# Kernel optimization log

Hardware: AMD Instinct MI355X
Metric: run time of the kernel (lower is better)

## Reference

```python
import jax, jax.numpy as jnp
import numpy as np

B, S, E, H = 1, 2048, 1024, 16
D = E // H
HEAVY_RATIO, RECENT_RATIO, PENALTY = 0.1, 0.1, 0.99
NEG = jnp.finfo(jnp.float32).min


def heavy_hitter_mask(attn, heavy_budget, recent_budget, penalty):
    # attn: [N, S, S] pre-softmax scores (with causal mask already added)
    N, Sq, _ = attn.shape
    cb = heavy_budget + recent_budget  # cache budget
    cols = jnp.arange(Sq)
    tmp = jax.nn.softmax(attn.astype(jnp.float32), axis=-1)
    # exponential penalty factor: penalty ** (cb-1, cb-2, ..., 0)
    pf = penalty ** (jnp.arange(cb, 0, -1).astype(jnp.float32) - 1.0)
    acc = jnp.einsum('nts,t->ns', tmp[:, :cb, :], pf)  # accumulated attention score [N,S]
    acc = acc * (cols < cb).astype(jnp.float32)        # zero beyond cache budget
    prev0 = jnp.broadcast_to(cols < cb, (N, Sq))       # mask_bottom row cb-1 (pre-tril)
    rows = jnp.swapaxes(attn[:, cb:, :], 0, 1)         # time-major [T,N,S]
    toks = jnp.arange(cb, Sq)

    def step(carry, inp):
        acc, prev = carry
        row, tok = inp
        li = tok - recent_budget                       # local_index
        in_local = (cols < li)[None, :]
        acc = jnp.where(in_local, acc * prev.astype(jnp.float32), acc)
        scores = jnp.where(in_local, acc, -jnp.inf)
        _, idx = jax.lax.top_k(scores, heavy_budget)   # heavy hitters [N,k]
        heavy = jnp.zeros((N, Sq), bool).at[jnp.arange(N)[:, None], idx].set(True)
        mask_row = heavy | (cols >= li)[None, :]
        p = jax.nn.softmax(jnp.where(mask_row, row.astype(jnp.float32), NEG), axis=-1)
        acc = acc * penalty + p
        # carry pre-tril row (matches torch loop); emit tril'd row
        return (acc, mask_row), mask_row & (cols <= tok)[None, :]

    (_, _), out_rows = jax.lax.scan(step, (acc, prev0), (rows, toks))
    # first cb rows: all-True cb x cb block, then tril -> causal within block
    top = jnp.broadcast_to((cols[None, :] <= jnp.arange(cb)[:, None])[None], (N, cb, Sq))
    return jnp.concatenate([top, jnp.swapaxes(out_rows, 0, 1)], axis=1)


def _forward(hidden_states, attention_mask, Wq, bq, Wk, bk, Wv, bv, Wo, bo):
    scaling = D ** -0.5
    q = (hidden_states @ Wq.T + bq) * scaling
    k = hidden_states @ Wk.T + bk
    v = hidden_states @ Wv.T + bv

    def shp(x):
        return x.reshape(B, S, H, D).transpose(0, 2, 1, 3).reshape(B * H, S, D)

    q, k, v = shp(q), shp(k), shp(v)
    attn = jnp.einsum('nsd,ntd->nst', q, k)                    # [B*H,S,S]
    attn = attn.reshape(B, H, S, S) + attention_mask
    attn = jnp.maximum(attn, NEG).reshape(B * H, S, S)
    hb = int(HEAVY_RATIO * S)
    rb = int(RECENT_RATIO * S)
    mask = heavy_hitter_mask(attn, hb, rb, PENALTY)
    attn = jnp.where(mask, attn, jnp.min(attention_mask))
    probs = jax.nn.softmax(attn.astype(jnp.float32), axis=-1)
    out = jnp.einsum('nst,ntd->nsd', probs, v)
    out = out.reshape(B, H, S, D).transpose(0, 2, 1, 3).reshape(B, S, E)
    return out @ Wo.T + bo


def setup_inputs() -> dict:
    key = jax.random.key(0)
    ks = jax.random.split(key, 9)
    hidden_states = jax.random.normal(ks[0], (B, S, E), jnp.float32)
    cols = jnp.arange(S)
    causal = (cols[None, :] <= cols[:, None])
    attention_mask = jnp.where(causal, 0.0, NEG)[None, None].astype(jnp.float32)
    attention_mask = jnp.broadcast_to(attention_mask, (B, 1, S, S)) + jnp.zeros((B, 1, S, S), jnp.float32)
    lin = lambda k: jax.random.normal(k, (E, E), jnp.float32) * 0.02
    return {
        'hidden_states': hidden_states,
        'attention_mask': attention_mask,
        'Wq': lin(ks[1]), 'bq': jnp.zeros((E,), jnp.float32),
        'Wk': lin(ks[2]), 'bk': jnp.zeros((E,), jnp.float32),
        'Wv': lin(ks[3]), 'bv': jnp.zeros((E,), jnp.float32),
        'Wo': lin(ks[4]), 'bo': jnp.zeros((E,), jnp.float32),
    }


def reference(hidden_states, attention_mask, Wq, bq, Wk, bk, Wv, bv, Wo, bo):
    return _forward(hidden_states, attention_mask, Wq, bq, Wk, bk, Wv, bv, Wo, bo)
```

## Files before the change

### kernel.cpp

```cpp
#include <hip/hip_runtime.h>

#define S_ 2048
#define E_ 1024
#define H_ 16
#define D_ 64
#define HB_ 204
#define RB_ 204
#define CB_ 408
#define NSCAN_ (S_ - CB_)
#define PEN_ 0.99f
#define NEGINF (-__builtin_huge_valf())
#define POSINF (__builtin_huge_valf())

typedef unsigned short u16;
typedef unsigned int u32;
typedef unsigned int u32x4 __attribute__((ext_vector_type(4)));

__device__ __forceinline__ float bf2f(u16 u) {
    union { u32 u; float f; } a; a.u = ((u32)u) << 16; return a.f;
}
__device__ __forceinline__ u16 f2bf(float f) {
    union { float f; u32 u; } a; a.f = f;
    u32 r = (a.u + 0x7FFFu + ((a.u >> 16) & 1u)) >> 16;
    return (u16)r;
}

#define DPPF(ID, V, CTRL, RMASK) \
    __int_as_float(__builtin_amdgcn_update_dpp(__float_as_int(ID), __float_as_int(V), CTRL, RMASK, 0xf, false))

__device__ __forceinline__ float wsum64_63(float v) {
    float t;
    t = DPPF(0.f, v, 0x111, 0xf); v += t;
    t = DPPF(0.f, v, 0x112, 0xf); v += t;
    t = DPPF(0.f, v, 0x114, 0xf); v += t;
    t = DPPF(0.f, v, 0x118, 0xf); v += t;
    t = DPPF(0.f, v, 0x142, 0xa); v += t;
    t = DPPF(0.f, v, 0x143, 0xc); v += t;
    return v;
}
__device__ __forceinline__ float wsum64(float v) {
    v = wsum64_63(v);
    return __int_as_float(__builtin_amdgcn_readlane(__float_as_int(v), 63));
}
template <int CTRL, int RMASK>
__device__ __forceinline__ double dmin_step(double v) {
    const int lo = __double2loint(v), hi = __double2hiint(v);
    const int slo = __builtin_amdgcn_update_dpp(0, lo, CTRL, RMASK, 0xf, false);
    const int shi = __builtin_amdgcn_update_dpp(0x7FF00000, hi, CTRL, RMASK, 0xf, false);
    return fmin(v, __hiloint2double(shi, slo));
}
__device__ __forceinline__ double wmind64(double v) {
    v = dmin_step<0x111, 0xf>(v);
    v = dmin_step<0x112, 0xf>(v);
    v = dmin_step<0x114, 0xf>(v);
    v = dmin_step<0x118, 0xf>(v);
    v = dmin_step<0x142, 0xa>(v);
    v = dmin_step<0x143, 0xc>(v);
    return v;
}

__global__ __launch_bounds__(256) void qkv_gemm(
    const float* __restrict__ X,
    const float* __restrict__ W0, const float* __restrict__ b0,
    const float* __restrict__ W1, const float* __restrict__ b1,
    const float* __restrict__ W2, const float* __restrict__ b2,
    float* __restrict__ Q, float* __restrict__ K, float* __restrict__ V)
{
    const int z = blockIdx.z;
    const float* W    = (z == 0) ? W0 : (z == 1) ? W1 : W2;
    const float* bias = (z == 0) ? b0 : (z == 1) ? b1 : b2;
    float* dst        = (z == 0) ? Q  : (z == 1) ? K  : V;
    const int o0 = blockIdx.x * 128, s0 = blockIdx.y * 128;
    __shared__ float As[16][132];
    __shared__ float Bs[16][132];
    const int tid = threadIdx.x;
    const int ty = tid >> 4, tx = tid & 15;
    const int r = tid >> 1, kq = (tid & 1) << 3;
    float acc[8][8] = {};
    for (int kb = 0; kb < E_; kb += 16) {
        float4 a0 = *(const float4*)&X[(size_t)(s0 + r) * E_ + kb + kq];
        float4 a1 = *(const float4*)&X[(size_t)(s0 + r) * E_ + kb + kq + 4];
        float4 w0 = *(const float4*)&W[(size_t)(o0 + r) * E_ + kb + kq];
        float4 w1 = *(const float4*)&W[(size_t)(o0 + r) * E_ + kb + kq + 4];
        __syncthreads();
        As[kq+0][r]=a0.x; As[kq+1][r]=a0.y; As[kq+2][r]=a0.z; As[kq+3][r]=a0.w;
        As[kq+4][r]=a1.x; As[kq+5][r]=a1.y; As[kq+6][r]=a1.z; As[kq+7][r]=a1.w;
        Bs[kq+0][r]=w0.x; Bs[kq+1][r]=w0.y; Bs[kq+2][r]=w0.z; Bs[kq+3][r]=w0.w;
        Bs[kq+4][r]=w1.x; Bs[kq+5][r]=w1.y; Bs[kq+6][r]=w1.z; Bs[kq+7][r]=w1.w;
        __syncthreads();
        #pragma unroll
        for (int kk = 0; kk < 16; ++kk) {
            float av[8], bv[8];
            *(float4*)&av[0] = *(const float4*)&As[kk][ty * 8];
            *(float4*)&av[4] = *(const float4*)&As[kk][ty * 8 + 4];
            *(float4*)&bv[0] = *(const float4*)&Bs[kk][tx * 8];
            *(float4*)&bv[4] = *(const float4*)&Bs[kk][tx * 8 + 4];
            #pragma unroll
            for (int i = 0; i < 8; ++i)
                #pragma unroll
                for (int j = 0; j < 8; ++j) acc[i][j] += av[i] * bv[j];
        }
    }
    #pragma unroll
    for (int i = 0; i < 8; ++i) {
        const int s = s0 + ty * 8 + i;
        #pragma unroll
        for (int jq = 0; jq < 2; ++jq) {
            const int o = o0 + tx * 8 + jq * 4;
            float4 v;
            v.x = acc[i][jq*4+0] + bias[o+0];
            v.y = acc[i][jq*4+1] + bias[o+1];
            v.z = acc[i][jq*4+2] + bias[o+2];
            v.w = acc[i][jq*4+3] + bias[o+3];
            if (z == 0) { v.x *= 0.125f; v.y *= 0.125f; v.z *= 0.125f; v.w *= 0.125f; }
            *(float4*)&dst[((size_t)(o >> 6) * S_ + s) * D_ + (o & 63)] = v;
        }
    }
}

__global__ __launch_bounds__(256) void proj_gemm(
    const float* __restrict__ X, const float* __restrict__ W,
    const float* __restrict__ bias, float* __restrict__ Y)
{
    const int o0 = blockIdx.x * 128, s0 = blockIdx.y * 128;
    __shared__ float As[16][132];
    __shared__ float Bs[16][132];
    const int tid = threadIdx.x;
    const int ty = tid >> 4, tx = tid & 15;
    const int r = tid >> 1, kq = (tid & 1) << 3;
    float acc[8][8] = {};
    for (int kb = 0; kb < E_; kb += 16) {
        float4 a0 = *(const float4*)&X[(size_t)(s0 + r) * E_ + kb + kq];
        float4 a1 = *(const float4*)&X[(size_t)(s0 + r) * E_ + kb + kq + 4];
        float4 w0 = *(const float4*)&W[(size_t)(o0 + r) * E_ + kb + kq];
        float4 w1 = *(const float4*)&W[(size_t)(o0 + r) * E_ + kb + kq + 4];
        __syncthreads();
        As[kq+0][r]=a0.x; As[kq+1][r]=a0.y; As[kq+2][r]=a0.z; As[kq+3][r]=a0.w;
        As[kq+4][r]=a1.x; As[kq+5][r]=a1.y; As[kq+6][r]=a1.z; As[kq+7][r]=a1.w;
        Bs[kq+0][r]=w0.x; Bs[kq+1][r]=w0.y; Bs[kq+2][r]=w0.z; Bs[kq+3][r]=w0.w;
        Bs[kq+4][r]=w1.x; Bs[kq+5][r]=w1.y; Bs[kq+6][r]=w1.z; Bs[kq+7][r]=w1.w;
        __syncthreads();
        #pragma unroll
        for (int kk = 0; kk < 16; ++kk) {
            float av[8], bv[8];
            *(float4*)&av[0] = *(const float4*)&As[kk][ty * 8];
            *(float4*)&av[4] = *(const float4*)&As[kk][ty * 8 + 4];
            *(float4*)&bv[0] = *(const float4*)&Bs[kk][tx * 8];
            *(float4*)&bv[4] = *(const float4*)&Bs[kk][tx * 8 + 4];
            #pragma unroll
            for (int i = 0; i < 8; ++i)
                #pragma unroll
                for (int j = 0; j < 8; ++j) acc[i][j] += av[i] * bv[j];
        }
    }
    #pragma unroll
    for (int i = 0; i < 8; ++i) {
        const int s = s0 + ty * 8 + i;
        #pragma unroll
        for (int jq = 0; jq < 2; ++jq) {
            const int o = o0 + tx * 8 + jq * 4;
            float4 v;
            v.x = acc[i][jq*4+0] + bias[o+0];
            v.y = acc[i][jq*4+1] + bias[o+1];
            v.z = acc[i][jq*4+2] + bias[o+2];
            v.w = acc[i][jq*4+3] + bias[o+3];
            *(float4*)&Y[(size_t)s * E_ + o] = v;
        }
    }
}

__global__ __launch_bounds__(256) void sc_gemm(const float* __restrict__ Q,
                                               const float* __restrict__ K,
                                               u16* __restrict__ Sc)
{
    const int h = blockIdx.z;
    const int jt = blockIdx.x, it = blockIdx.y;
    if (jt > it) return;
    const int i0 = it * 64, j0 = jt * 64;
    __shared__ float Qs[64][65];
    __shared__ float Ks[64][65];
    const float* Qh = Q + (size_t)h * S_ * D_;
    const float* Kh = K + (size_t)h * S_ * D_;
    const int tid = threadIdx.x;
    for (int idx = tid; idx < 1024; idx += 256) {
        const int rr = idx >> 4, c4 = (idx & 15) << 2;
        float4 q4 = *(const float4*)&Qh[(size_t)(i0 + rr) * D_ + c4];
        Qs[c4 + 0][rr] = q4.x; Qs[c4 + 1][rr] = q4.y; Qs[c4 + 2][rr] = q4.z; Qs[c4 + 3][rr] = q4.w;
        float4 k4 = *(const float4*)&Kh[(size_t)(j0 + rr) * D_ + c4];
        Ks[c4 + 0][rr] = k4.x; Ks[c4 + 1][rr] = k4.y; Ks[c4 + 2][rr] = k4.z; Ks[c4 + 3][rr] = k4.w;
    }
    __syncthreads();
    const int ty = tid >> 4, tx = tid & 15;
    float acc[4][4] = {};
    #pragma unroll 4
    for (int kk = 0; kk < 64; ++kk) {
        float4 a4 = *(const float4*)&Qs[kk][ty * 4];
        float4 b4 = *(const float4*)&Ks[kk][tx * 4];
        const float av[4] = {a4.x, a4.y, a4.z, a4.w};
        const float bv[4] = {b4.x, b4.y, b4.z, b4.w};
        #pragma unroll
        for (int i = 0; i < 4; ++i)
            #pragma unroll
            for (int j = 0; j < 4; ++j) acc[i][j] += av[i] * bv[j];
    }
    u16* out = Sc + ((size_t)h * S_ + i0) * S_ + j0;
    #pragma unroll
    for (int i = 0; i < 4; ++i)
        #pragma unroll
        for (int j = 0; j < 4; ++j)
            out[(size_t)(ty * 4 + i) * S_ + tx * 4 + j] = f2bf(acc[i][j]);
}

__global__ __launch_bounds__(256) void prep_kernel(const u16* __restrict__ Sc,
                                                   float* __restrict__ rsumG,
                                                   float* __restrict__ accG)
{
    const int h = blockIdx.y;
    const int wave = threadIdx.x >> 6, lane = threadIdx.x & 63;
    const int bx = blockIdx.x;
    if (bx < NSCAN_ / 4) {
        const int tok = CB_ + bx * 4 + wave;
        const u16* row = Sc + ((size_t)h * S_ + tok) * S_ + (tok - RB_);
        float sm = 0.f;
        #pragma unroll
        for (int k = 0; k < 4; ++k) {
            const int j = k * 64 + lane;
            if (j <= RB_) sm += __expf(bf2f(row[j]));
        }
        const float z = wsum64(sm);
        if (lane == 0) rsumG[(size_t)h * NSCAN_ + tok - CB_] = z;
    } else {
        const int t = (bx - NSCAN_ / 4) * 4 + wave;
        const u16* row = Sc + ((size_t)h * S_ + t) * S_;
        float sm = 0.f;
        for (int c = lane; c <= t; c += 64) sm += __expf(bf2f(row[c]));
        const float z = wsum64(sm);
        const float w = __powf(PEN_, (float)(CB_ - 1 - t)) / z;
        for (int c = lane; c <= t; c += 64)
            atomicAdd(&accG[h * CB_ + c], __expf(bf2f(row[c])) * w);
    }
}

#define NFULL_ (CB_ * H_)
#define NPART_ (NSCAN_ * H_)

__global__ __launch_bounds__(256) void scan_fill(const u16* __restrict__ Sc,
                                                 const float* __restrict__ accG,
                                                 const float* __restrict__ rsumG,
                                                 u16* __restrict__ heavyOut,
                                                 const float* __restrict__ V,
                                                 float* __restrict__ O)
{
    __shared__ __align__(16) char ldsPool[15872];
    const int bid = blockIdx.x;
    const int tid = threadIdx.x;

    if (bid >= 16) {
        float* sbuf  = (float*)ldsPool;
        float* wred  = (float*)(ldsPool + 1664);
        float* opart = (float*)(ldsPool + 1696);
        const int lane = tid & 63, wave = tid >> 6;
        int h, r, c0, n;
        bool partial;
        if (bid < 16 + NFULL_) {
            const int t2 = bid - 16;
            r = t2 >> 4; h = t2 & 15;
            c0 = 0; n = r + 1; partial = false;
        } else {
            const int idx = bid - 16 - NFULL_;
            r = CB_ + (idx >> 4); h = idx & 15;
            c0 = r - RB_; n = RB_ + 1; partial = true;
        }
        const u16* srow = Sc + ((size_t)h * S_ + r) * S_;
        float ls = 0.f;
        for (int i = tid; i < n; i += 256) {
            const float p = __expf(bf2f(srow[c0 + i]));
            sbuf[i] = p; ls += p;
        }
        ls = wsum64(ls);
        if (lane == 0) wred[wave] = ls;
        __syncthreads();
        const float Z = wred[0] + wred[1] + wred[2] + wred[3];
        float pv = 0.f;
        const float* vh = V + (size_t)h * S_ * D_;
        for (int i = wave; i < n; i += 4)
            pv += sbuf[i] * vh[(size_t)(c0 + i) * D_ + lane];
        opart[wave * 64 + lane] = pv;
        __syncthreads();
        if (tid < 64) {
            const float tot = opart[tid] + opart[64 + tid] + opart[128 + tid] + opart[192 + tid];
            O[(size_t)r * E_ + h * D_ + tid] = partial ? tot : (tot / Z);
        }
        return;
    }

    __builtin_amdgcn_s_setprio(3);
    const int h = bid;
    const int lane = tid & 63, wv = tid >> 6;
    float*  ring    = (float*)ldsPool;
    float*  rsumLDS = (float*)(ldsPool + 1024);
    u16*    rowbufA = (u16*)(ldsPool + 7584);
    u16*    rowbufB = (u16*)(ldsPool + 11680);
    float*  wredL   = (float*)(ldsPool + 15776);
    double* kredL   = (double*)(ldsPool + 15792);
    float*  eli1L   = (float*)(ldsPool + 15824);
    const u16* sch = Sc + (size_t)h * S_ * S_;
    const float* accH = accG + h * CB_;
    u16* hOutH = heavyOut + (size_t)h * NSCAN_ * HB_;

    const bool vHeavy = (tid < HB_);
    const bool vRing  = (tid <= RB_);
    const bool vCand  = (tid == 255);

    u32x4 p0, p1, p2, p3;
    #define ISSUE1(BUF, ROWI)                                                 \
        do {                                                                  \
            const void* _ap = (const void*)((const char*)(sch + (size_t)(ROWI) * S_) + tid * 16); \
            asm volatile("global_load_dwordx4 %0, %1, off"                    \
                         : "=&v"(BUF) : "v"(_ap) : "memory");                 \
        } while (0)
    #define WAIT_VM(N) asm volatile("s_waitcnt vmcnt(" #N ")" ::: "memory")
    #define SBAR() asm volatile("s_waitcnt lgkmcnt(0)\n\ts_barrier" ::: "memory")

    ISSUE1(p0, CB_ + 0);
    ISSUE1(p1, CB_ + 1);
    ISSUE1(p2, CB_ + 2);
    ISSUE1(p3, CB_ + 3);

    for (int i = tid; i < NSCAN_; i += 256) rsumLDS[i] = rsumG[(size_t)h * NSCAN_ + i];
    for (int c = HB_ + tid; c < CB_; c += 256) ring[c & 255] = accH[c];
    int   hcol = vHeavy ? tid : 0;
    float hacc = vHeavy ? accH[tid] : POSINF;

    __syncthreads();
    ((u32x4*)rowbufA)[tid] = p0;
    __syncthreads();

    {
        ISSUE1(p0, CB_ + 4);
        const u16* srow = rowbufA;
        const float sg = bf2f(srow[hcol]);
        const float e  = vHeavy ? __expf(sg) : 0.f;
        const float ls = wsum64_63(e);
        if (lane == 63) wredL[wv] = ls;
        float oldw = 0.f, expw = 0.f;
        if (vRing) {
            expw = __expf(bf2f(srow[HB_ + tid]));
            oldw = (tid == RB_) ? 0.f : ring[(HB_ + tid) & 255];
        }
        ((u32x4*)rowbufB)[tid] = p1;
        __syncthreads();
        const float4 ws = *(const float4*)wredL;
        const float Z = ws.x + ws.y + ws.z + ws.w + rsumLDS[0];
        const float invZ = __fdividef(1.f, Z);
        hacc = hacc * PEN_ + e * invZ;
        if (vHeavy) hOutH[tid] = (u16)tid;
        if (vRing)  ring[(HB_ + tid) & 255] = oldw * PEN_ + expw * invZ;
        __syncthreads();
    }

    #define SCAN_ITER(TOK, LD, ST, WN, FS)                                       \
    do {                                                                         \
        const int _si_tok = (TOK);                                               \
        const int _si_li  = _si_tok - RB_;                                       \
        const int _si_nr  = (_si_tok + 4 < S_) ? _si_tok + 4 : S_ - 1;           \
        ISSUE1(LD, _si_nr);                                                      \
        const u16* _si_srow = (_si_tok & 1) ? rowbufB : rowbufA;                 \
        const float _si_accc = ring[(_si_li - 1) & 255];      \
        const int   _si_hc = vCand ? (_si_li - 1) : hcol;                        \
        const float _si_ha = vCand ? _si_accc : hacc;                            \
        const float _si_sg = bf2f(_si_srow[_si_hc]);                             \
        float _si_oldw = 0.f, _si_expw = 0.f;                                    \
        if (vRing) {                                                             \
            _si_expw = __expf(bf2f(_si_srow[_si_li + tid]));                     \
            _si_oldw = (tid == RB_) ? 0.f : ring[(_si_li + tid) & 255];          \
        }                                                                        \
        const float _si_rsum = rsumLDS[_si_tok - CB_];                           \
        const float _si_e = (vHeavy || vCand) ? __expf(_si_sg) : 0.f;            \
        const float _si_ls = wsum64_63(_si_e);                                   \
        double _si_key = __hiloint2double(__float_as_int(_si_ha),                \
                                          ((2047 - _si_hc) << 8) | tid);         \
        _si_key = wmind64(_si_key);                                              \
        if (lane == 63) {                                                        \
            wredL[wv] = _si_ls;                                                  \
            kredL[wv] = _si_key;                                                 \
            if (wv == 3) *eli1L = _si_e;                                         \
        }                                                                        \
        if (!(FS)) { WAIT_VM(WN); }                                              \
        ((u32x4*)(((_si_tok + 1) & 1) ? rowbufB : rowbufA))[tid] = (ST);         \
        if (FS) { __syncthreads(); } else { SBAR(); }                            \
        const float4 _si_ws = *(const float4*)wredL;                             \
        const double _si_km = fmin(fmin(kredL[0], kredL[1]),                     \
                                   fmin(kredL[2], kredL[3]));                    \
        const int _si_lo  = __double2loint(_si_km);                              \
        const int _si_ev  = _si_lo & 255;                                        \
        const int _si_hev = 2047 - (_si_lo >> 8);                                \
        const float _si_ebc = __expf(bf2f(_si_srow[_si_hev]));                   \
        const float _si_el1 = *eli1L;                                            \
        const float _si_Z = (_si_ws.x + _si_ws.y + _si_ws.z + _si_ws.w)          \
                            - _si_ebc + _si_rsum;                                \
        const float _si_invZ = __fdividef(1.f, _si_Z);                           \
        const bool _si_m = (tid == _si_ev);                                      \
        hcol = _si_m ? (_si_li - 1) : _si_hc;                                    \
        hacc = (_si_m ? _si_accc : _si_ha) * PEN_                                \
             + (_si_m ? _si_el1 : _si_e) * _si_invZ;                             \
        if (vHeavy) hOutH[(size_t)(_si_tok - CB_) * HB_ + tid] = (u16)hcol;      \
        if (vRing)  ring[(_si_li + tid) & 255] = _si_oldw * PEN_ + _si_expw * _si_invZ; \
        if (FS) { __syncthreads(); } else { SBAR(); }                            \
    } while (0)

    SCAN_ITER(CB_ + 1, p1, p2, 0, 1);
    SCAN_ITER(CB_ + 2, p2, p3, 0, 1);
    SCAN_ITER(CB_ + 3, p3, p0, 0, 1);
    SCAN_ITER(CB_ + 4, p0, p1, 3, 0);
    for (int tokBase = CB_ + 5; tokBase + 3 < S_; tokBase += 4) {
        SCAN_ITER(tokBase + 0, p1, p2, 3, 0);
        SCAN_ITER(tokBase + 1, p2, p3, 3, 0);
        SCAN_ITER(tokBase + 2, p3, p0, 3, 0);
        SCAN_ITER(tokBase + 3, p0, p1, 3, 0);
    }
    SCAN_ITER(S_ - 3, p1, p2, 3, 0);
    SCAN_ITER(S_ - 2, p2, p3, 3, 0);
    SCAN_ITER(S_ - 1, p3, p0, 3, 0);
    #undef SCAN_ITER
    #undef ISSUE1
    #undef WAIT_VM
    #undef SBAR
}

__global__ __launch_bounds__(256) void heavy_merge(const u16* __restrict__ Sc,
                                                   const float* __restrict__ V,
                                                   const u16* __restrict__ heavyIn,
                                                   const float* __restrict__ rsumG,
                                                   float* __restrict__ O)
{
    const int idx = blockIdx.x;
    const int r = CB_ + (idx >> 4), h = idx & 15;
    const int tid = threadIdx.x;
    const int lane = tid & 63, wave = tid >> 6;
    __shared__ float sbuf[208];
    __shared__ u16 cbuf[208];
    __shared__ float wred[4];
    __shared__ float opart[4][64];
    const u16* srow = Sc + ((size_t)h * S_ + r) * S_;
    const u16* hrow = heavyIn + ((size_t)h * NSCAN_ + (r - CB_)) * HB_;
    float ls = 0.f;
    for (int i = tid; i < HB_; i += 256) {
        const int col = hrow[i];
        const float p = __expf(bf2f(srow[col]));
        sbuf[i] = p; cbuf[i] = (u16)col;
        ls += p;
    }
    ls = wsum64(ls);
    if (lane == 0) wred[wave] = ls;
    __syncthreads();
    const float Z = wred[0] + wred[1] + wred[2] + wred[3]
                  + rsumG[(size_t)h * NSCAN_ + r - CB_];
    float pv = 0.f;
    const float* vh = V + (size_t)h * S_ * D_;
    for (int i = wave; i < HB_; i += 4)
        pv += sbuf[i] * vh[(size_t)cbuf[i] * D_ + lane];
    opart[wave][lane] = pv;
    __syncthreads();
    if (tid < 64) {
        const float tot = opart[0][tid] + opart[1][tid] + opart[2][tid] + opart[3][tid];
        float* op = &O[(size_t)r * E_ + h * D_ + tid];
        *op = (*op + tot) / Z;
    }
}

extern "C" void kernel_launch(void* const* d_in, const int* in_sizes, int n_in,
                              void* d_out, int out_size, void* d_ws, size_t ws_size,
                              hipStream_t stream)
{
    const float* hs = (const float*)d_in[0];
    const float* Wq = (const float*)d_in[2];
    const float* bq = (const float*)d_in[3];
    const float* Wk = (const float*)d_in[4];
    const float* bk = (const float*)d_in[5];
    const float* Wv = (const float*)d_in[6];
    const float* bv = (const float*)d_in[7];
    const float* Wo = (const float*)d_in[8];
    const float* bo = (const float*)d_in[9];

    char* ws = (char*)d_ws;
    const size_t MB = 1024 * 1024;
    float* Q     = (float*)(ws);
    float* K     = (float*)(ws + 8 * MB);
    float* V     = (float*)(ws + 16 * MB);
    u16*   Sc    = (u16*)  (ws + 24 * MB);
    u16*   hvy   = (u16*)  (ws + 152 * MB);
    float* rsumG = (float*)(ws + 163 * MB);
    float* accG  = (float*)(ws + 164 * MB);
    float* O     = (float*)(ws + 168 * MB);
    (void)ws_size; (void)in_sizes; (void)n_in; (void)out_size;

    (void)hipMemsetAsync(accG, 0, (size_t)H_ * CB_ * sizeof(float), stream);
    qkv_gemm<<<dim3(8, 16, 3), 256, 0, stream>>>(hs, Wq, bq, Wk, bk, Wv, bv, Q, K, V);
    sc_gemm <<<dim3(32, 32, 16), 256, 0, stream>>>(Q, K, Sc);
    prep_kernel<<<dim3(NSCAN_ / 4 + CB_ / 4, H_), 256, 0, stream>>>(Sc, rsumG, accG);
    scan_fill<<<16 + NFULL_ + NPART_, 256, 0, stream>>>(Sc, accG, rsumG, hvy, V, O);
    heavy_merge<<<NPART_, 256, 0, stream>>>(Sc, V, hvy, rsumG, O);
    proj_gemm<<<dim3(8, 16, 1), 256, 0, stream>>>(O, Wo, bo, (float*)d_out);
}
```

Measured before the change: 1.640 ms.

## Remove second barrier per scan step via triple-buffered rows and parity reduction slots

The sequential heavy-hitter scan now uses three LDS row buffers and two alternating reduction slots, so each token step needs one barrier instead of two. The candidate accumulator for the column leaving the recent window is carried in a register rather than reread from the ring after a barrier, and ring updates are reordered so they cannot race with the next step's reads. This targets barrier latency on the serial critical path of the scan, at the cost of more LDS and subtler ordering that must hold across steps.

Measured after the change: 1.637 ms. About the same (-0.2%).

```diff
diff --git a/kernel.cpp b/kernel.cpp
--- a/kernel.cpp
+++ b/kernel.cpp
@@ -251,7 +251,7 @@
                                                  const float* __restrict__ V,
                                                  float* __restrict__ O)
 {
-    __shared__ __align__(16) char ldsPool[15872];
+    __shared__ __align__(16) char ldsPool[19984];
     const int bid = blockIdx.x;
     const int tid = threadIdx.x;
 
@@ -299,11 +299,12 @@
     const int lane = tid & 63, wv = tid >> 6;
     float*  ring    = (float*)ldsPool;
     float*  rsumLDS = (float*)(ldsPool + 1024);
-    u16*    rowbufA = (u16*)(ldsPool + 7584);
-    u16*    rowbufB = (u16*)(ldsPool + 11680);
-    float*  wredL   = (float*)(ldsPool + 15776);
-    double* kredL   = (double*)(ldsPool + 15792);
-    float*  eli1L   = (float*)(ldsPool + 15824);
+    u16*    buf_0   = (u16*)(ldsPool + 7584);
+    u16*    buf_1   = (u16*)(ldsPool + 11680);
+    u16*    buf_2   = (u16*)(ldsPool + 15776);
+    float*  wredL   = (float*)(ldsPool + 19872);
+    double* kredL   = (double*)(ldsPool + 19904);
+    float*  el1L    = (float*)(ldsPool + 19968);
     const u16* sch = Sc + (size_t)h * S_ * S_;
     const float* accH = accG + h * CB_;
     u16* hOutH = heavyOut + (size_t)h * NSCAN_ * HB_;
@@ -331,14 +332,15 @@
     for (int c = HB_ + tid; c < CB_; c += 256) ring[c & 255] = accH[c];
     int   hcol = vHeavy ? tid : 0;
     float hacc = vHeavy ? accH[tid] : POSINF;
+    float accc;
 
     __syncthreads();
-    ((u32x4*)rowbufA)[tid] = p0;
+    ((u32x4*)buf_0)[tid] = p0;
     __syncthreads();
 
     {
         ISSUE1(p0, CB_ + 4);
-        const u16* srow = rowbufA;
+        const u16* srow = buf_0;
         const float sg = bf2f(srow[hcol]);
         const float e  = vHeavy ? __expf(sg) : 0.f;
         const float ls = wsum64_63(e);
@@ -348,7 +350,7 @@
             expw = __expf(bf2f(srow[HB_ + tid]));
             oldw = (tid == RB_) ? 0.f : ring[(HB_ + tid) & 255];
         }
-        ((u32x4*)rowbufB)[tid] = p1;
+        ((u32x4*)buf_1)[tid] = p1;
         __syncthreads();
         const float4 ws = *(const float4*)wredL;
         const float Z = ws.x + ws.y + ws.z + ws.w + rsumLDS[0];
@@ -357,71 +359,81 @@
         if (vHeavy) hOutH[tid] = (u16)tid;
         if (vRing)  ring[(HB_ + tid) & 255] = oldw * PEN_ + expw * invZ;
         __syncthreads();
-    }
-
-    #define SCAN_ITER(TOK, LD, ST, WN, FS)                                       \
+        accc = ring[HB_ & 255];
+    }
+
+    #define SCAN_ITER(TOK, LD, ST, SB, DB, P)                                    \
     do {                                                                         \
         const int _si_tok = (TOK);                                               \
         const int _si_li  = _si_tok - RB_;                                       \
         const int _si_nr  = (_si_tok + 4 < S_) ? _si_tok + 4 : S_ - 1;           \
         ISSUE1(LD, _si_nr);                                                      \
-        const u16* _si_srow = (_si_tok & 1) ? rowbufB : rowbufA;                 \
-        const float _si_accc = ring[(_si_li - 1) & 255];      \
+        const u16* _si_srow = buf_##SB;                                          \
         const int   _si_hc = vCand ? (_si_li - 1) : hcol;                        \
-        const float _si_ha = vCand ? _si_accc : hacc;                            \
+        const float _si_ha = vCand ? accc : hacc;                                \
         const float _si_sg = bf2f(_si_srow[_si_hc]);                             \
-        float _si_oldw = 0.f, _si_expw = 0.f;                                    \
-        if (vRing) {                                                             \
-            _si_expw = __expf(bf2f(_si_srow[_si_li + tid]));                     \
-            _si_oldw = (tid == RB_) ? 0.f : ring[(_si_li + tid) & 255];          \
-        }                                                                        \
-        const float _si_rsum = rsumLDS[_si_tok - CB_];                           \
+        float _si_expw = 0.f;                                                    \
+        if (vRing) _si_expw = __expf(bf2f(_si_srow[_si_li + tid]));              \
         const float _si_e = (vHeavy || vCand) ? __expf(_si_sg) : 0.f;            \
         const float _si_ls = wsum64_63(_si_e);                                   \
         double _si_key = __hiloint2double(__float_as_int(_si_ha),                \
                                           ((2047 - _si_hc) << 8) | tid);         \
         _si_key = wmind64(_si_key);                                              \
         if (lane == 63) {                                                        \
-            wredL[wv] = _si_ls;                                                  \
-            kredL[wv] = _si_key;                                                 \
-            if (wv == 3) *eli1L = _si_e;                                         \
+            wredL[(P) * 4 + wv] = _si_ls;                                        \
+            kredL[(P) * 4 + wv] = _si_key;                                       \
+            if (wv == 3) el1L[P] = _si_e;                                        \
         }                                                                        \
-        if (!(FS)) { WAIT_VM(WN); }                                              \
-        ((u32x4*)(((_si_tok + 1) & 1) ? rowbufB : rowbufA))[tid] = (ST);         \
-        if (FS) { __syncthreads(); } else { SBAR(); }                            \
-        const float4 _si_ws = *(const float4*)wredL;                             \
-        const double _si_km = fmin(fmin(kredL[0], kredL[1]),                     \
-                                   fmin(kredL[2], kredL[3]));                    \
+        WAIT_VM(3);                                                              \
+        ((u32x4*)buf_##DB)[tid] = (ST);                                          \
+        SBAR();                                                                  \
+        const float4 _si_ws = *(const float4*)&wredL[(P) * 4];                   \
+        const double _si_km = fmin(fmin(kredL[(P)*4+0], kredL[(P)*4+1]),         \
+                                   fmin(kredL[(P)*4+2], kredL[(P)*4+3]));        \
         const int _si_lo  = __double2loint(_si_km);                              \
         const int _si_ev  = _si_lo & 255;                                        \
         const int _si_hev = 2047 - (_si_lo >> 8);                                \
         const float _si_ebc = __expf(bf2f(_si_srow[_si_hev]));                   \
-        const float _si_el1 = *eli1L;                                            \
+        const float _si_el1 = el1L[P];                                           \
+        const float _si_rsum = rsumLDS[_si_tok - CB_];                           \
         const float _si_Z = (_si_ws.x + _si_ws.y + _si_ws.z + _si_ws.w)          \
                             - _si_ebc + _si_rsum;                                \
         const float _si_invZ = __fdividef(1.f, _si_Z);                           \
+        const float _si_oldw0 = ring[_si_li & 255];                              \
+        if (vRing && tid != 0) {                                                 \
+            const float _si_oldw = (tid == RB_) ? 0.f : ring[(_si_li + tid) & 255]; \
+            ring[(_si_li + tid) & 255] = _si_oldw * PEN_ + _si_expw * _si_invZ;  \
+        }                                                                        \
         const bool _si_m = (tid == _si_ev);                                      \
         hcol = _si_m ? (_si_li - 1) : _si_hc;                                    \
-        hacc = (_si_m ? _si_accc : _si_ha) * PEN_                                \
+        hacc = (_si_m ? accc : _si_ha) * PEN_                                    \
              + (_si_m ? _si_el1 : _si_e) * _si_invZ;                             \
+        const float _si_ew0 = __expf(bf2f(_si_srow[_si_li]));                    \
+        accc = _si_oldw0 * PEN_ + _si_ew0 * _si_invZ;                            \
         if (vHeavy) hOutH[(size_t)(_si_tok - CB_) * HB_ + tid] = (u16)hcol;      \
-        if (vRing)  ring[(_si_li + tid) & 255] = _si_oldw * PEN_ + _si_expw * _si_invZ; \
-        if (FS) { __syncthreads(); } else { SBAR(); }                            \
     } while (0)
 
-    SCAN_ITER(CB_ + 1, p1, p2, 0, 1);
-    SCAN_ITER(CB_ + 2, p2, p3, 0, 1);
-    SCAN_ITER(CB_ + 3, p3, p0, 0, 1);
-    SCAN_ITER(CB_ + 4, p0, p1, 3, 0);
-    for (int tokBase = CB_ + 5; tokBase + 3 < S_; tokBase += 4) {
-        SCAN_ITER(tokBase + 0, p1, p2, 3, 0);
-        SCAN_ITER(tokBase + 1, p2, p3, 3, 0);
-        SCAN_ITER(tokBase + 2, p3, p0, 3, 0);
-        SCAN_ITER(tokBase + 3, p0, p1, 3, 0);
-    }
-    SCAN_ITER(S_ - 3, p1, p2, 3, 0);
-    SCAN_ITER(S_ - 2, p2, p3, 3, 0);
-    SCAN_ITER(S_ - 1, p3, p0, 3, 0);
+    SCAN_ITER(CB_ + 1, p1, p2, 1, 2, 1);
+    SCAN_ITER(CB_ + 2, p2, p3, 2, 0, 0);
+    SCAN_ITER(CB_ + 3, p3, p0, 0, 1, 1);
+    SCAN_ITER(CB_ + 4, p0, p1, 1, 2, 0);
+    for (int t = CB_ + 5; t + 11 <= S_ - 4; t += 12) {
+        SCAN_ITER(t + 0,  p1, p2, 2, 0, 1);
+        SCAN_ITER(t + 1,  p2, p3, 0, 1, 0);
+        SCAN_ITER(t + 2,  p3, p0, 1, 2, 1);
+        SCAN_ITER(t + 3,  p0, p1, 2, 0, 0);
+        SCAN_ITER(t + 4,  p1, p2, 0, 1, 1);
+        SCAN_ITER(t + 5,  p2, p3, 1, 2, 0);
+        SCAN_ITER(t + 6,  p3, p0, 2, 0, 1);
+        SCAN_ITER(t + 7,  p0, p1, 0, 1, 0);
+        SCAN_ITER(t + 8,  p1, p2, 1, 2, 1);
+        SCAN_ITER(t + 9,  p2, p3, 2, 0, 0);
+        SCAN_ITER(t + 10, p3, p0, 0, 1, 1);
+        SCAN_ITER(t + 11, p0, p1, 1, 2, 0);
+    }
+    SCAN_ITER(S_ - 3, p1, p2, 2, 0, 1);
+    SCAN_ITER(S_ - 2, p2, p3, 0, 1, 0);
+    SCAN_ITER(S_ - 1, p3, p0, 1, 2, 1);
     #undef SCAN_ITER
     #undef ISSUE1
     #undef WAIT_VM
```
